# Performance work log

Hardware: AMD Instinct MI355X
Metric: run time of the kernel (lower is better)

## Reference

```python
import jax, jax.numpy as jnp
import numpy as np
import math

VOCAB, N_LAYERS, D_MODEL, D_K, D_V, D_FF, N_HEADS = 32000, 2, 1024, 64, 64, 4096, 16
B, L = 4, 1024
EPS = 1e-5


def _layer_norm(x):
    # LayerNorm over last dim, elementwise_affine=False, eps=1e-5
    mu = jnp.mean(x, axis=-1, keepdims=True)
    var = jnp.var(x, axis=-1, keepdims=True)
    return (x - mu) * jax.lax.rsqrt(var + EPS)


def _sinusoidal_pe(max_len, d_model):
    pos = np.arange(max_len, dtype=np.float32)[:, None]
    div = np.exp(np.arange(0, d_model, 2, dtype=np.float32) * (-math.log(10000.0) / d_model))
    pe = np.zeros((max_len, d_model), dtype=np.float32)
    pe[:, 0::2] = np.sin(pos * div)
    pe[:, 1::2] = np.cos(pos * div)
    return jnp.asarray(pe)


def setup_inputs() -> dict:
    key = jax.random.key(0)
    ks = jax.random.split(key, 8)
    s = lambda fan_in: 1.0 / np.sqrt(fan_in)
    enc_inputs = jax.random.randint(ks[0], (B, L), 0, VOCAB, dtype=jnp.int32)
    emb = jax.random.normal(ks[1], (VOCAB, D_MODEL), dtype=jnp.float32)
    pe = _sinusoidal_pe(L, D_MODEL)
    WQ = jax.random.normal(ks[2], (N_LAYERS, D_MODEL, N_HEADS * D_K), dtype=jnp.float32) * s(D_MODEL)
    WK = jax.random.normal(ks[3], (N_LAYERS, D_MODEL, N_HEADS * D_K), dtype=jnp.float32) * s(D_MODEL)
    WV = jax.random.normal(ks[4], (N_LAYERS, D_MODEL, N_HEADS * D_V), dtype=jnp.float32) * s(D_MODEL)
    WO = jax.random.normal(ks[5], (N_LAYERS, N_HEADS * D_V, D_MODEL), dtype=jnp.float32) * s(N_HEADS * D_V)
    W1 = jax.random.normal(ks[6], (N_LAYERS, D_MODEL, D_FF), dtype=jnp.float32) * s(D_MODEL)
    W2 = jax.random.normal(ks[7], (N_LAYERS, D_FF, D_MODEL), dtype=jnp.float32) * s(D_FF)
    return {"enc_inputs": enc_inputs, "emb": emb, "pe": pe, "WQ": WQ, "WK": WK, "WV": WV, "WO": WO, "W1": W1, "W2": W2}


def reference(enc_inputs, emb, pe, WQ, WK, WV, WO, W1, W2):
    b, l = enc_inputs.shape
    n_layers = WQ.shape[0]
    x = emb[enc_inputs] + pe[:l]  # [b,l,d]
    # pad mask: True where key token == 0; broadcast over heads and queries
    pad = (enc_inputs == 0)[:, None, None, :]  # [b,1,1,lk]
    scale = 1.0 / math.sqrt(D_K)
    attns = []
    for i in range(n_layers):
        q = (x @ WQ[i]).reshape(b, l, N_HEADS, D_K).transpose(0, 2, 1, 3)  # [b,h,l,dk]
        k = (x @ WK[i]).reshape(b, l, N_HEADS, D_K).transpose(0, 2, 1, 3)
        v = (x @ WV[i]).reshape(b, l, N_HEADS, D_V).transpose(0, 2, 1, 3)
        scores = jnp.einsum('bhqd,bhkd->bhqk', q, k) * scale
        scores = jnp.where(pad, -1e9, scores)
        a = jax.nn.softmax(scores, axis=-1)  # [b,h,l,l]
        ctx = jnp.einsum('bhqk,bhkd->bhqd', a, v)
        ctx = ctx.transpose(0, 2, 1, 3).reshape(b, l, N_HEADS * D_V)
        x = _layer_norm(ctx @ WO[i] + x)
        x = _layer_norm(jax.nn.relu(x @ W1[i]) @ W2[i] + x)
        attns.append(a)
    return x, jnp.stack(attns)
```

## Files before the change

kernel.cpp:

```cpp
#include <hip/hip_runtime.h>
#include <hip/hip_bf16.h>
#include <math.h>

#define BATCH 4
#define SEQ 1024
#define DMODEL 1024
#define NHEADS 16
#define DHEAD 64
#define DFFDIM 4096
#define NLAYERS 2
#define MTOT (BATCH*SEQ)

typedef __hip_bfloat16 bf16;
typedef float f32x4 __attribute__((ext_vector_type(4)));
typedef short bf16x8 __attribute__((ext_vector_type(8)));

__device__ __forceinline__ unsigned short bfbits(float f) {
  bf16 h = __float2bfloat16(f);
  return *(unsigned short*)&h;
}

__global__ __launch_bounds__(256) void k_embed(const int* __restrict__ ids,
                                               const float* __restrict__ emb,
                                               const float* __restrict__ pe,
                                               float* __restrict__ x,
                                               bf16* __restrict__ xb) {
  int row = blockIdx.x;
  int l = row & (SEQ - 1);
  int tok = ids[row];
  const float4* e = (const float4*)(emb + (size_t)tok * DMODEL);
  const float4* p = (const float4*)(pe + (size_t)l * DMODEL);
  float4* o = (float4*)(x + (size_t)row * DMODEL);
  int i = threadIdx.x;
  float4 a = e[i], c = p[i];
  float4 r = make_float4(a.x + c.x, a.y + c.y, a.z + c.z, a.w + c.w);
  o[i] = r;
  ushort4 u;
  u.x = bfbits(r.x); u.y = bfbits(r.y); u.z = bfbits(r.z); u.w = bfbits(r.w);
  *(ushort4*)(xb + (size_t)row * DMODEL + i * 4) = u;
}

__global__ __launch_bounds__(256) void k_wcvt(const float* __restrict__ W,
                                              bf16* __restrict__ Wt,
                                              int Kdim, int Ndim) {
  __shared__ float t[32][33];
  const float* Ws = W + (size_t)blockIdx.z * Kdim * Ndim;
  bf16* Wd = Wt + (size_t)blockIdx.z * Kdim * Ndim;
  int n0 = blockIdx.x * 32, k0 = blockIdx.y * 32;
  int tx = threadIdx.x & 31, ty = threadIdx.x >> 5;
#pragma unroll
  for (int j = 0; j < 32; j += 8)
    t[ty + j][tx] = Ws[(size_t)(k0 + ty + j) * Ndim + n0 + tx];
  __syncthreads();
#pragma unroll
  for (int j = 0; j < 32; j += 8)
    Wd[(size_t)(n0 + ty + j) * Kdim + k0 + tx] = __float2bfloat16(t[tx][ty + j]);
}

template<int MODE>
__global__ __launch_bounds__(256) void k_mfma_gemm(const bf16* __restrict__ A,
                                                   const bf16* __restrict__ Bt,
                                                   void* __restrict__ C,
                                                   int Mdim, int Ndim, int Kdim) {
  __shared__ __align__(16) short As[128 * 32];
  __shared__ __align__(16) short Bs[128 * 32];
  const int tid = threadIdx.x;
  const int wave = tid >> 6, lane = tid & 63;
  const int l15 = lane & 15, l4 = lane >> 4;
  const int row0 = blockIdx.y * 128, col0 = blockIdx.x * 128;
  const int wr = wave >> 1, wc = wave & 1;

  f32x4 acc[4][4] = {};

  for (int k0 = 0; k0 < Kdim; k0 += 32) {
#pragma unroll
    for (int i = 0; i < 2; ++i) {
      int c = i * 256 + tid;
      int r = c >> 2, kc = (c & 3) * 8;
      const bf16* ga = A + (size_t)(row0 + r) * Kdim + k0 + kc;
      char* la = (char*)As + (i * 256 + wave * 64) * 16;
      __builtin_amdgcn_global_load_lds((const __attribute__((address_space(1))) void*)ga,
                                       (__attribute__((address_space(3))) void*)la, 16, 0, 0);
      const bf16* gb = Bt + (size_t)(col0 + r) * Kdim + k0 + kc;
      char* lb = (char*)Bs + (i * 256 + wave * 64) * 16;
      __builtin_amdgcn_global_load_lds((const __attribute__((address_space(1))) void*)gb,
                                       (__attribute__((address_space(3))) void*)lb, 16, 0, 0);
    }
    __syncthreads();
    bf16x8 af[4], bfr[4];
#pragma unroll
    for (int m = 0; m < 4; ++m)
      af[m] = *(const bf16x8*)&As[(wr * 64 + m * 16 + l15) * 32 + l4 * 8];
#pragma unroll
    for (int n = 0; n < 4; ++n)
      bfr[n] = *(const bf16x8*)&Bs[(wc * 64 + n * 16 + l15) * 32 + l4 * 8];
#pragma unroll
    for (int m = 0; m < 4; ++m)
#pragma unroll
      for (int n = 0; n < 4; ++n)
        acc[m][n] = __builtin_amdgcn_mfma_f32_16x16x32_bf16(af[m], bfr[n], acc[m][n], 0, 0, 0);
    __syncthreads();
  }

#pragma unroll
  for (int m = 0; m < 4; ++m) {
#pragma unroll
    for (int n = 0; n < 4; ++n) {
      int col = col0 + wc * 64 + n * 16 + l15;
#pragma unroll
      for (int j = 0; j < 4; ++j) {
        int row = row0 + wr * 64 + m * 16 + l4 * 4 + j;
        float v = acc[m][n][j];
        if (MODE == 2) v = fmaxf(v, 0.f);
        if (MODE == 0)
          ((float*)C)[(size_t)row * Ndim + col] = v;
        else
          ((bf16*)C)[(size_t)row * Ndim + col] = __float2bfloat16(v);
      }
    }
  }
}

__global__ __launch_bounds__(256) void k_scores(const bf16* __restrict__ q,
                                                const bf16* __restrict__ k,
                                                const int* __restrict__ ids,
                                                float* __restrict__ attn) {
  __shared__ float Qs[64][65];
  __shared__ float Ks[64][65];
  int bh = blockIdx.z;
  int b = bh >> 4, h = bh & 15;
  int row0 = blockIdx.y * 64, col0 = blockIdx.x * 64;
  const bf16* qb = q + (size_t)b * SEQ * DMODEL + h * DHEAD;
  const bf16* kb = k + (size_t)b * SEQ * DMODEL + h * DHEAD;
  for (int i = threadIdx.x; i < 4096; i += 256) {
    int r = i >> 6, c = i & 63;
    Qs[r][c] = __bfloat162float(qb[(size_t)(row0 + r) * DMODEL + c]);
    Ks[r][c] = __bfloat162float(kb[(size_t)(col0 + r) * DMODEL + c]);
  }
  __syncthreads();
  int tx = threadIdx.x & 15, ty = threadIdx.x >> 4;
  float acc[4][4] = {};
#pragma unroll 8
  for (int d = 0; d < 64; ++d) {
    float a[4], bb[4];
#pragma unroll
    for (int i = 0; i < 4; ++i) a[i] = Qs[ty * 4 + i][d];
#pragma unroll
    for (int j = 0; j < 4; ++j) bb[j] = Ks[tx * 4 + j][d];
#pragma unroll
    for (int i = 0; i < 4; ++i)
#pragma unroll
      for (int j = 0; j < 4; ++j)
        acc[i][j] = fmaf(a[i], bb[j], acc[i][j]);
  }
  float* ob = attn + (size_t)bh * SEQ * SEQ;
#pragma unroll
  for (int j = 0; j < 4; ++j) {
    int col = col0 + tx * 4 + j;
    bool msk = (ids[b * SEQ + col] == 0);
#pragma unroll
    for (int i = 0; i < 4; ++i) {
      float v = msk ? -1e9f : acc[i][j] * 0.125f;
      ob[(size_t)(row0 + ty * 4 + i) * SEQ + col] = v;
    }
  }
}

__global__ __launch_bounds__(256) void k_softmax(float* __restrict__ a) {
  int row = blockIdx.x * 4 + (threadIdx.x >> 6);
  int lane = threadIdx.x & 63;
  float4* p = (float4*)(a + (size_t)row * SEQ);
  float4 v[4];
  float mx = -3e38f;
#pragma unroll
  for (int i = 0; i < 4; ++i) {
    v[i] = p[lane + 64 * i];
    mx = fmaxf(mx, fmaxf(fmaxf(v[i].x, v[i].y), fmaxf(v[i].z, v[i].w)));
  }
#pragma unroll
  for (int off = 32; off > 0; off >>= 1) mx = fmaxf(mx, __shfl_xor(mx, off, 64));
  float s = 0.f;
#pragma unroll
  for (int i = 0; i < 4; ++i) {
    v[i].x = __expf(v[i].x - mx); v[i].y = __expf(v[i].y - mx);
    v[i].z = __expf(v[i].z - mx); v[i].w = __expf(v[i].w - mx);
    s += v[i].x + v[i].y + v[i].z + v[i].w;
  }
#pragma unroll
  for (int off = 32; off > 0; off >>= 1) s += __shfl_xor(s, off, 64);
  float inv = 1.f / s;
#pragma unroll
  for (int i = 0; i < 4; ++i) {
    v[i].x *= inv; v[i].y *= inv; v[i].z *= inv; v[i].w *= inv;
    p[lane + 64 * i] = v[i];
  }
}

__global__ __launch_bounds__(256) void k_pv(const float* __restrict__ attn,
                                            const bf16* __restrict__ v,
                                            bf16* __restrict__ ctx) {
  __shared__ float As_[16][65];
  __shared__ float Bs_[16][65];
  int bh = blockIdx.y;
  int b = bh >> 4, h = bh & 15;
  int row0 = blockIdx.x * 64;
  const float* ab = attn + (size_t)bh * SEQ * SEQ;
  const bf16* vb = v + (size_t)b * SEQ * DMODEL + h * DHEAD;
  int tx = threadIdx.x & 15, ty = threadIdx.x >> 4;
  float acc[4][4] = {};
  for (int k0 = 0; k0 < SEQ; k0 += 16) {
    for (int i = threadIdx.x; i < 1024; i += 256) {
      int m = i >> 4, kk = i & 15;
      As_[kk][m] = ab[(size_t)(row0 + m) * SEQ + (k0 + kk)];
      int kk2 = i >> 6, n = i & 63;
      Bs_[kk2][n] = __bfloat162float(vb[(size_t)(k0 + kk2) * DMODEL + n]);
    }
    __syncthreads();
#pragma unroll
    for (int kk = 0; kk < 16; ++kk) {
      float a[4], bb[4];
#pragma unroll
      for (int i = 0; i < 4; ++i) a[i] = As_[kk][ty * 4 + i];
#pragma unroll
      for (int j = 0; j < 4; ++j) bb[j] = Bs_[kk][tx * 4 + j];
#pragma unroll
      for (int i = 0; i < 4; ++i)
#pragma unroll
        for (int j = 0; j < 4; ++j)
          acc[i][j] = fmaf(a[i], bb[j], acc[i][j]);
    }
    __syncthreads();
  }
  bf16* ob = ctx + (size_t)b * SEQ * DMODEL + h * DHEAD;
#pragma unroll
  for (int i = 0; i < 4; ++i) {
    ushort4 u;
    u.x = bfbits(acc[i][0]); u.y = bfbits(acc[i][1]);
    u.z = bfbits(acc[i][2]); u.w = bfbits(acc[i][3]);
    *(ushort4*)&ob[(size_t)(row0 + ty * 4 + i) * DMODEL + tx * 4] = u;
  }
}

__global__ __launch_bounds__(256) void k_addln(const float* __restrict__ t,
                                               const float* __restrict__ xin,
                                               float* __restrict__ xout,
                                               bf16* __restrict__ xbout) {
  int row = blockIdx.x * 4 + (threadIdx.x >> 6);
  int lane = threadIdx.x & 63;
  const float4* tp = (const float4*)(t + (size_t)row * DMODEL);
  const float4* xp = (const float4*)(xin + (size_t)row * DMODEL);
  float4* op = (float4*)(xout + (size_t)row * DMODEL);
  bf16* bp = xbout + (size_t)row * DMODEL;
  float4 v[4];
  float s = 0.f;
#pragma unroll
  for (int i = 0; i < 4; ++i) {
    float4 a = tp[lane + 64 * i], c = xp[lane + 64 * i];
    v[i] = make_float4(a.x + c.x, a.y + c.y, a.z + c.z, a.w + c.w);
    s += v[i].x + v[i].y + v[i].z + v[i].w;
  }
#pragma unroll
  for (int off = 32; off > 0; off >>= 1) s += __shfl_xor(s, off, 64);
  float mu = s * (1.f / DMODEL);
  float ss = 0.f;
#pragma unroll
  for (int i = 0; i < 4; ++i) {
    float dx = v[i].x - mu, dy = v[i].y - mu, dz = v[i].z - mu, dw = v[i].w - mu;
    ss += dx * dx + dy * dy + dz * dz + dw * dw;
  }
#pragma unroll
  for (int off = 32; off > 0; off >>= 1) ss += __shfl_xor(ss, off, 64);
  float r = rsqrtf(ss * (1.f / DMODEL) + 1e-5f);
#pragma unroll
  for (int i = 0; i < 4; ++i) {
    float4 o = make_float4((v[i].x - mu) * r, (v[i].y - mu) * r,
                           (v[i].z - mu) * r, (v[i].w - mu) * r);
    op[lane + 64 * i] = o;
    ushort4 u;
    u.x = bfbits(o.x); u.y = bfbits(o.y); u.z = bfbits(o.z); u.w = bfbits(o.w);
    *(ushort4*)&bp[(lane + 64 * i) * 4] = u;
  }
}

extern "C" void kernel_launch(void* const* d_in, const int* in_sizes, int n_in,
                              void* d_out, int out_size, void* d_ws, size_t ws_size,
                              hipStream_t stream) {
  const int*   ids = (const int*)d_in[0];
  const float* emb = (const float*)d_in[1];
  const float* pe  = (const float*)d_in[2];
  const float* WQ  = (const float*)d_in[3];
  const float* WK  = (const float*)d_in[4];
  const float* WV  = (const float*)d_in[5];
  const float* WO  = (const float*)d_in[6];
  const float* W1  = (const float*)d_in[7];
  const float* W2  = (const float*)d_in[8];
  float* out = (float*)d_out;

  const size_t MB = 1024 * 1024;
  char* ws = (char*)d_ws;
  float* x   = (float*)(ws);
  float* t   = (float*)(ws + 16 * MB);
  bf16*  xb  = (bf16*)(ws + 32 * MB);
  bf16*  qb  = (bf16*)(ws + 40 * MB);
  bf16*  kb  = (bf16*)(ws + 48 * MB);
  bf16*  vb  = (bf16*)(ws + 56 * MB);
  bf16*  hb  = (bf16*)(ws + 64 * MB);
  bf16*  wqt = (bf16*)(ws + 96 * MB);
  bf16*  wkt = (bf16*)(ws + 100 * MB);
  bf16*  wvt = (bf16*)(ws + 104 * MB);
  bf16*  wot = (bf16*)(ws + 108 * MB);
  bf16*  w1t = (bf16*)(ws + 112 * MB);
  bf16*  w2t = (bf16*)(ws + 128 * MB);

  k_wcvt<<<dim3(DMODEL / 32, DMODEL / 32, NLAYERS), 256, 0, stream>>>(WQ, wqt, DMODEL, DMODEL);
  k_wcvt<<<dim3(DMODEL / 32, DMODEL / 32, NLAYERS), 256, 0, stream>>>(WK, wkt, DMODEL, DMODEL);
  k_wcvt<<<dim3(DMODEL / 32, DMODEL / 32, NLAYERS), 256, 0, stream>>>(WV, wvt, DMODEL, DMODEL);
  k_wcvt<<<dim3(DMODEL / 32, DMODEL / 32, NLAYERS), 256, 0, stream>>>(WO, wot, DMODEL, DMODEL);
  k_wcvt<<<dim3(DFFDIM / 32, DMODEL / 32, NLAYERS), 256, 0, stream>>>(W1, w1t, DMODEL, DFFDIM);
  k_wcvt<<<dim3(DMODEL / 32, DFFDIM / 32, NLAYERS), 256, 0, stream>>>(W2, w2t, DFFDIM, DMODEL);

  k_embed<<<MTOT, 256, 0, stream>>>(ids, emb, pe, x, xb);

  for (int layer = 0; layer < NLAYERS; ++layer) {
    const bf16* lwq = wqt + (size_t)layer * DMODEL * DMODEL;
    const bf16* lwk = wkt + (size_t)layer * DMODEL * DMODEL;
    const bf16* lwv = wvt + (size_t)layer * DMODEL * DMODEL;
    const bf16* lwo = wot + (size_t)layer * DMODEL * DMODEL;
    const bf16* lw1 = w1t + (size_t)layer * DMODEL * DFFDIM;
    const bf16* lw2 = w2t + (size_t)layer * DFFDIM * DMODEL;

    dim3 gq(DMODEL / 128, MTOT / 128);
    k_mfma_gemm<1><<<gq, 256, 0, stream>>>(xb, lwq, qb, MTOT, DMODEL, DMODEL);
    k_mfma_gemm<1><<<gq, 256, 0, stream>>>(xb, lwk, kb, MTOT, DMODEL, DMODEL);
    k_mfma_gemm<1><<<gq, 256, 0, stream>>>(xb, lwv, vb, MTOT, DMODEL, DMODEL);

    float* attn = out + (size_t)MTOT * DMODEL + (size_t)layer * BATCH * NHEADS * SEQ * SEQ;
    dim3 gs(SEQ / 64, SEQ / 64, BATCH * NHEADS);
    k_scores<<<gs, 256, 0, stream>>>(qb, kb, ids, attn);
    k_softmax<<<BATCH * NHEADS * SEQ / 4, 256, 0, stream>>>(attn);
    dim3 gp(SEQ / 64, BATCH * NHEADS);
    k_pv<<<gp, 256, 0, stream>>>(attn, vb, qb);

    k_mfma_gemm<0><<<gq, 256, 0, stream>>>(qb, lwo, t, MTOT, DMODEL, DMODEL);
    k_addln<<<MTOT / 4, 256, 0, stream>>>(t, x, x, xb);

    dim3 g1(DFFDIM / 128, MTOT / 128);
    k_mfma_gemm<2><<<g1, 256, 0, stream>>>(xb, lw1, hb, MTOT, DFFDIM, DMODEL);
    dim3 g2(DMODEL / 128, MTOT / 128);
    k_mfma_gemm<0><<<g2, 256, 0, stream>>>(hb, lw2, t, MTOT, DMODEL, DFFDIM);

    float* xo = (layer == NLAYERS - 1) ? out : x;
    k_addln<<<MTOT / 4, 256, 0, stream>>>(t, x, xo, xb);
  }
}
```

Before: 2.192 ms.

## Move attention QK^T and PV onto bf16 MFMA with swizzled LDS tiles

```diff
diff --git a/kernel.cpp b/kernel.cpp
--- a/kernel.cpp
+++ b/kernel.cpp
@@ -57,6 +57,21 @@
     Wd[(size_t)(n0 + ty + j) * Kdim + k0 + tx] = __float2bfloat16(t[tx][ty + j]);
 }
 
+__global__ __launch_bounds__(256) void k_vt(const bf16* __restrict__ v,
+                                            bf16* __restrict__ vt) {
+  __shared__ short t[32][33];
+  int bh = blockIdx.z, b = bh >> 4, h = bh & 15;
+  int l0 = blockIdx.x * 32, d0 = blockIdx.y * 32;
+  int tx = threadIdx.x & 31, ty = threadIdx.x >> 5;
+#pragma unroll
+  for (int j = 0; j < 32; j += 8)
+    t[ty + j][tx] = *(const short*)&v[(size_t)(b * SEQ + l0 + ty + j) * DMODEL + h * DHEAD + d0 + tx];
+  __syncthreads();
+#pragma unroll
+  for (int j = 0; j < 32; j += 8)
+    *(short*)&vt[((size_t)bh * DHEAD + d0 + ty + j) * SEQ + l0 + tx] = t[tx][ty + j];
+}
+
 template<int MODE>
 __global__ __launch_bounds__(256) void k_mfma_gemm(const bf16* __restrict__ A,
                                                    const bf16* __restrict__ Bt,
@@ -121,55 +136,76 @@
   }
 }
 
-__global__ __launch_bounds__(256) void k_scores(const bf16* __restrict__ q,
-                                                const bf16* __restrict__ k,
-                                                const int* __restrict__ ids,
-                                                float* __restrict__ attn) {
-  __shared__ float Qs[64][65];
-  __shared__ float Ks[64][65];
-  int bh = blockIdx.z;
-  int b = bh >> 4, h = bh & 15;
-  int row0 = blockIdx.y * 64, col0 = blockIdx.x * 64;
+__global__ __launch_bounds__(256) void k_scores_mfma(const bf16* __restrict__ q,
+                                                     const bf16* __restrict__ kin,
+                                                     const int* __restrict__ ids,
+                                                     float* __restrict__ attn) {
+  __shared__ __align__(16) char As[128 * 128];
+  __shared__ __align__(16) char Bs[128 * 128];
+  const int tid = threadIdx.x;
+  const int wave = tid >> 6;
+  const int lane = tid & 63;
+  const int l15 = lane & 15, l4 = lane >> 4;
+  const int bh = blockIdx.z, b = bh >> 4, h = bh & 15;
+  const int row0 = blockIdx.y * 128, col0 = blockIdx.x * 128;
+  const int wr = wave >> 1, wc = wave & 1;
   const bf16* qb = q + (size_t)b * SEQ * DMODEL + h * DHEAD;
-  const bf16* kb = k + (size_t)b * SEQ * DMODEL + h * DHEAD;
-  for (int i = threadIdx.x; i < 4096; i += 256) {
-    int r = i >> 6, c = i & 63;
-    Qs[r][c] = __bfloat162float(qb[(size_t)(row0 + r) * DMODEL + c]);
-    Ks[r][c] = __bfloat162float(kb[(size_t)(col0 + r) * DMODEL + c]);
+  const bf16* kb = kin + (size_t)b * SEQ * DMODEL + h * DHEAD;
+#pragma unroll
+  for (int i = 0; i < 4; ++i) {
+    int c = i * 256 + tid;
+    int r = c >> 3;
+    int kc = ((c ^ r) & 7) * 8;
+    __builtin_amdgcn_global_load_lds(
+        (const __attribute__((address_space(1))) void*)(qb + (size_t)(row0 + r) * DMODEL + kc),
+        (__attribute__((address_space(3))) void*)(As + (size_t)(i * 256 + wave * 64) * 16), 16, 0, 0);
+    __builtin_amdgcn_global_load_lds(
+        (const __attribute__((address_space(1))) void*)(kb + (size_t)(col0 + r) * DMODEL + kc),
+        (__attribute__((address_space(3))) void*)(Bs + (size_t)(i * 256 + wave * 64) * 16), 16, 0, 0);
   }
   __syncthreads();
-  int tx = threadIdx.x & 15, ty = threadIdx.x >> 4;
-  float acc[4][4] = {};
-#pragma unroll 8
-  for (int d = 0; d < 64; ++d) {
-    float a[4], bb[4];
-#pragma unroll
-    for (int i = 0; i < 4; ++i) a[i] = Qs[ty * 4 + i][d];
-#pragma unroll
-    for (int j = 0; j < 4; ++j) bb[j] = Ks[tx * 4 + j][d];
-#pragma unroll
-    for (int i = 0; i < 4; ++i)
-#pragma unroll
-      for (int j = 0; j < 4; ++j)
-        acc[i][j] = fmaf(a[i], bb[j], acc[i][j]);
+  f32x4 acc[4][4] = {};
+#pragma unroll
+  for (int kk = 0; kk < 2; ++kk) {
+    bf16x8 af[4], bfr[4];
+    int j = l4 + kk * 4;
+#pragma unroll
+    for (int m = 0; m < 4; ++m) {
+      int row = wr * 64 + m * 16 + l15;
+      af[m] = *(const bf16x8*)(As + row * 128 + ((j ^ (row & 7)) * 16));
+    }
+#pragma unroll
+    for (int n = 0; n < 4; ++n) {
+      int row = wc * 64 + n * 16 + l15;
+      bfr[n] = *(const bf16x8*)(Bs + row * 128 + ((j ^ (row & 7)) * 16));
+    }
+#pragma unroll
+    for (int m = 0; m < 4; ++m)
+#pragma unroll
+      for (int n = 0; n < 4; ++n)
+        acc[m][n] = __builtin_amdgcn_mfma_f32_16x16x32_bf16(af[m], bfr[n], acc[m][n], 0, 0, 0);
   }
   float* ob = attn + (size_t)bh * SEQ * SEQ;
 #pragma unroll
-  for (int j = 0; j < 4; ++j) {
-    int col = col0 + tx * 4 + j;
+  for (int n = 0; n < 4; ++n) {
+    int col = col0 + wc * 64 + n * 16 + l15;
     bool msk = (ids[b * SEQ + col] == 0);
 #pragma unroll
-    for (int i = 0; i < 4; ++i) {
-      float v = msk ? -1e9f : acc[i][j] * 0.125f;
-      ob[(size_t)(row0 + ty * 4 + i) * SEQ + col] = v;
-    }
-  }
-}
-
-__global__ __launch_bounds__(256) void k_softmax(float* __restrict__ a) {
+    for (int m = 0; m < 4; ++m)
+#pragma unroll
+      for (int j = 0; j < 4; ++j) {
+        int row = row0 + wr * 64 + m * 16 + l4 * 4 + j;
+        ob[(size_t)row * SEQ + col] = msk ? -1e9f : acc[m][n][j] * 0.125f;
+      }
+  }
+}
+
+__global__ __launch_bounds__(256) void k_softmax(float* __restrict__ a,
+                                                 bf16* __restrict__ ab) {
   int row = blockIdx.x * 4 + (threadIdx.x >> 6);
   int lane = threadIdx.x & 63;
   float4* p = (float4*)(a + (size_t)row * SEQ);
+  bf16* bp = ab + (size_t)row * SEQ;
   float4 v[4];
   float mx = -3e38f;
 #pragma unroll
@@ -193,52 +229,75 @@
   for (int i = 0; i < 4; ++i) {
     v[i].x *= inv; v[i].y *= inv; v[i].z *= inv; v[i].w *= inv;
     p[lane + 64 * i] = v[i];
-  }
-}
-
-__global__ __launch_bounds__(256) void k_pv(const float* __restrict__ attn,
-                                            const bf16* __restrict__ v,
-                                            bf16* __restrict__ ctx) {
-  __shared__ float As_[16][65];
-  __shared__ float Bs_[16][65];
-  int bh = blockIdx.y;
-  int b = bh >> 4, h = bh & 15;
-  int row0 = blockIdx.x * 64;
-  const float* ab = attn + (size_t)bh * SEQ * SEQ;
-  const bf16* vb = v + (size_t)b * SEQ * DMODEL + h * DHEAD;
-  int tx = threadIdx.x & 15, ty = threadIdx.x >> 4;
-  float acc[4][4] = {};
-  for (int k0 = 0; k0 < SEQ; k0 += 16) {
-    for (int i = threadIdx.x; i < 1024; i += 256) {
-      int m = i >> 4, kk = i & 15;
-      As_[kk][m] = ab[(size_t)(row0 + m) * SEQ + (k0 + kk)];
-      int kk2 = i >> 6, n = i & 63;
-      Bs_[kk2][n] = __bfloat162float(vb[(size_t)(k0 + kk2) * DMODEL + n]);
+    ushort4 u;
+    u.x = bfbits(v[i].x); u.y = bfbits(v[i].y); u.z = bfbits(v[i].z); u.w = bfbits(v[i].w);
+    *(ushort4*)&bp[(lane + 64 * i) * 4] = u;
+  }
+}
+
+__global__ __launch_bounds__(256) void k_pv_mfma(const bf16* __restrict__ pb,
+                                                 const bf16* __restrict__ vt,
+                                                 bf16* __restrict__ ctx) {
+  __shared__ __align__(16) char As[128 * 128];
+  __shared__ __align__(16) char Bs[64 * 128];
+  const int tid = threadIdx.x;
+  const int wave = tid >> 6, lane = tid & 63;
+  const int l15 = lane & 15, l4 = lane >> 4;
+  const int bh = blockIdx.y, b = bh >> 4, h = bh & 15;
+  const int row0 = blockIdx.x * 128;
+  const bf16* arow = pb + (size_t)bh * SEQ * SEQ + (size_t)row0 * SEQ;
+  const bf16* vrow = vt + (size_t)bh * DHEAD * SEQ;
+  f32x4 acc[2][4] = {};
+  for (int k0 = 0; k0 < SEQ; k0 += 64) {
+#pragma unroll
+    for (int i = 0; i < 4; ++i) {
+      int c = i * 256 + tid;
+      int r = c >> 3, kc = ((c ^ r) & 7) * 8;
+      __builtin_amdgcn_global_load_lds(
+          (const __attribute__((address_space(1))) void*)(arow + (size_t)r * SEQ + k0 + kc),
+          (__attribute__((address_space(3))) void*)(As + (size_t)(i * 256 + wave * 64) * 16), 16, 0, 0);
+    }
+#pragma unroll
+    for (int i = 0; i < 2; ++i) {
+      int c = i * 256 + tid;
+      int r = c >> 3, kc = ((c ^ r) & 7) * 8;
+      __builtin_amdgcn_global_load_lds(
+          (const __attribute__((address_space(1))) void*)(vrow + (size_t)r * SEQ + k0 + kc),
+          (__attribute__((address_space(3))) void*)(Bs + (size_t)(i * 256 + wave * 64) * 16), 16, 0, 0);
     }
     __syncthreads();
 #pragma unroll
-    for (int kk = 0; kk < 16; ++kk) {
-      float a[4], bb[4];
-#pragma unroll
-      for (int i = 0; i < 4; ++i) a[i] = As_[kk][ty * 4 + i];
-#pragma unroll
-      for (int j = 0; j < 4; ++j) bb[j] = Bs_[kk][tx * 4 + j];
-#pragma unroll
-      for (int i = 0; i < 4; ++i)
-#pragma unroll
-        for (int j = 0; j < 4; ++j)
-          acc[i][j] = fmaf(a[i], bb[j], acc[i][j]);
+    for (int kk = 0; kk < 2; ++kk) {
+      bf16x8 af[2], bfr[4];
+      int j = l4 + kk * 4;
+#pragma unroll
+      for (int m = 0; m < 2; ++m) {
+        int row = wave * 32 + m * 16 + l15;
+        af[m] = *(const bf16x8*)(As + row * 128 + ((j ^ (row & 7)) * 16));
+      }
+#pragma unroll
+      for (int n = 0; n < 4; ++n) {
+        int row = n * 16 + l15;
+        bfr[n] = *(const bf16x8*)(Bs + row * 128 + ((j ^ (row & 7)) * 16));
+      }
+#pragma unroll
+      for (int m = 0; m < 2; ++m)
+#pragma unroll
+        for (int n = 0; n < 4; ++n)
+          acc[m][n] = __builtin_amdgcn_mfma_f32_16x16x32_bf16(af[m], bfr[n], acc[m][n], 0, 0, 0);
     }
     __syncthreads();
   }
   bf16* ob = ctx + (size_t)b * SEQ * DMODEL + h * DHEAD;
 #pragma unroll
-  for (int i = 0; i < 4; ++i) {
-    ushort4 u;
-    u.x = bfbits(acc[i][0]); u.y = bfbits(acc[i][1]);
-    u.z = bfbits(acc[i][2]); u.w = bfbits(acc[i][3]);
-    *(ushort4*)&ob[(size_t)(row0 + ty * 4 + i) * DMODEL + tx * 4] = u;
-  }
+  for (int m = 0; m < 2; ++m)
+#pragma unroll
+    for (int n = 0; n < 4; ++n)
+#pragma unroll
+      for (int j = 0; j < 4; ++j) {
+        int row = row0 + wave * 32 + m * 16 + l4 * 4 + j;
+        ob[(size_t)row * DMODEL + n * 16 + l15] = __float2bfloat16(acc[m][n][j]);
+      }
 }
 
 __global__ __launch_bounds__(256) void k_addln(const float* __restrict__ t,
@@ -311,6 +370,8 @@
   bf16*  wot = (bf16*)(ws + 108 * MB);
   bf16*  w1t = (bf16*)(ws + 112 * MB);
   bf16*  w2t = (bf16*)(ws + 128 * MB);
+  bf16*  vt  = (bf16*)(ws + 144 * MB);
+  bf16*  pb  = (bf16*)(ws + 152 * MB);
 
   k_wcvt<<<dim3(DMODEL / 32, DMODEL / 32, NLAYERS), 256, 0, stream>>>(WQ, wqt, DMODEL, DMODEL);
   k_wcvt<<<dim3(DMODEL / 32, DMODEL / 32, NLAYERS), 256, 0, stream>>>(WK, wkt, DMODEL, DMODEL);
@@ -334,12 +395,14 @@
     k_mfma_gemm<1><<<gq, 256, 0, stream>>>(xb, lwk, kb, MTOT, DMODEL, DMODEL);
     k_mfma_gemm<1><<<gq, 256, 0, stream>>>(xb, lwv, vb, MTOT, DMODEL, DMODEL);
 
+    k_vt<<<dim3(SEQ / 32, DHEAD / 32, BATCH * NHEADS), 256, 0, stream>>>(vb, vt);
+
     float* attn = out + (size_t)MTOT * DMODEL + (size_t)layer * BATCH * NHEADS * SEQ * SEQ;
-    dim3 gs(SEQ / 64, SEQ / 64, BATCH * NHEADS);
-    k_scores<<<gs, 256, 0, stream>>>(qb, kb, ids, attn);
-    k_softmax<<<BATCH * NHEADS * SEQ / 4, 256, 0, stream>>>(attn);
-    dim3 gp(SEQ / 64, BATCH * NHEADS);
-    k_pv<<<gp, 256, 0, stream>>>(attn, vb, qb);
+    dim3 gs(SEQ / 128, SEQ / 128, BATCH * NHEADS);
+    k_scores_mfma<<<gs, 256, 0, stream>>>(qb, kb, ids, attn);
+    k_softmax<<<BATCH * NHEADS * SEQ / 4, 256, 0, stream>>>(attn, pb);
+    dim3 gp(SEQ / 128, BATCH * NHEADS);
+    k_pv_mfma<<<gp, 256, 0, stream>>>(pb, vt, qb);
 
     k_mfma_gemm<0><<<gq, 256, 0, stream>>>(qb, lwo, t, MTOT, DMODEL, DMODEL);
     k_addln<<<MTOT / 4, 256, 0, stream>>>(t, x, x, xb);
```

Measured after the change: 1.768 ms. 1.24x faster.
